# Kernel tuning notes

Hardware: AMD Instinct MI355X
Metric: run time of the kernel (lower is better)

## Reference

```python
import jax, jax.numpy as jnp
import numpy as np

BATCH = 16384
XD = 64      # x_dim
AD = 16      # a_dim
NC = 8       # number of constraints
PEN = 10.0   # relax_penalty
DELTA = 1.0  # class-K coefficient
ITERS = 250  # FISTA iterations for the dual QP (converges to OSQP solution)


def _cbf_forward(a_des, x, A, B, Qc, cc, dc):
    """Batched CBF-QP safety filter.

    Constraints: g_i(x) = 0.5 x^T Qc_i x + cc_i^T x - dc_i  (g_i <= 0 is safe)
    Barrier:     h_i(x) = -g_i(x),  grad_h = -(Qc_i x + cc_i)
    QP:  min ||a - a_des||^2 + PEN * ||s||^2
         s.t. Lg_h a >= -Lf_h - DELTA*h - s,  s >= 0
    Solved exactly (to FISTA tolerance) via the dual:
         min_{lam>=0} 0.5 lam^T M lam - lam^T q,
    with z = [a; s], H = diag(2*1_AD, 2*PEN*1_NC), z = z0 + H^{-1} G^T lam.
    """
    bsz = a_des.shape[0]
    # constraint values and gradients (the 'autograd jacobian' in the original)
    g_x = 0.5 * jnp.einsum('bi,mij,bj->bm', x, Qc, x) + x @ cc.T - dc[None, :]
    h_x = -g_x                                              # [B, NC]
    grad_h = -(jnp.einsum('mij,bj->bmi', Qc, x) + cc[None])  # [B, NC, XD]
    # Lie derivatives
    Lf_h = jnp.einsum('bmi,bij,bj->bm', grad_h, A, x)        # [B, NC]
    Lg_h = jnp.einsum('bmi,bia->bma', grad_h, B)             # [B, NC, AD]
    bvec = -Lf_h - DELTA * h_x                               # rhs: Lg_h a + s >= bvec

    # dual QP setup: G z >= c, G = [[Lg_h, I],[0, I]], c = [bvec; 0]
    Im = jnp.broadcast_to(jnp.eye(NC, dtype=a_des.dtype), (bsz, NC, NC))
    Gtop = jnp.concatenate([Lg_h, Im], axis=2)                    # [B, NC, AD+NC]
    Gbot = jnp.concatenate([jnp.zeros((bsz, NC, AD), a_des.dtype), Im], axis=2)
    G = jnp.concatenate([Gtop, Gbot], axis=1)                     # [B, 2NC, AD+NC]
    dinv = jnp.concatenate([0.5 * jnp.ones(AD, a_des.dtype),
                            jnp.ones(NC, a_des.dtype) / (2.0 * PEN)])
    Mmat = jnp.einsum('bkn,n,bln->bkl', G, dinv, G)               # [B, 2NC, 2NC]
    q = jnp.concatenate([bvec - jnp.einsum('bma,ba->bm', Lg_h, a_des),
                         jnp.zeros((bsz, NC), a_des.dtype)], axis=1)

    # step size 1/L, L = max eigenvalue of M (not differentiated)
    L = jax.lax.stop_gradient(jnp.linalg.eigvalsh(Mmat)[..., -1]) + 1e-6
    t = (1.0 / L)[:, None]

    lam0 = jnp.zeros((bsz, 2 * NC), a_des.dtype)

    def step(carry, _):
        lam, y, tk = carry
        grad = jnp.einsum('bkl,bl->bk', Mmat, y) - q
        lam_new = jnp.maximum(y - t * grad, 0.0)
        tk1 = 0.5 * (1.0 + jnp.sqrt(1.0 + 4.0 * tk * tk))
        y_new = lam_new + ((tk - 1.0) / tk1) * (lam_new - lam)
        return (lam_new, y_new, tk1), None

    (lam, _, _), _ = jax.lax.scan(step, (lam0, lam0, jnp.float32(1.0)), None, length=ITERS)

    # primal recovery: a = a_des + 0.5 * Lg_h^T lam_top
    a_safe = a_des + 0.5 * jnp.einsum('bma,bm->ba', Lg_h, lam[:, :NC])
    return a_safe


def setup_inputs() -> dict:
    key = jax.random.key(0)
    ks = jax.random.split(key, 7)
    a_des = jax.random.normal(ks[0], (BATCH, AD), jnp.float32)
    x = jax.random.normal(ks[1], (BATCH, XD), jnp.float32)
    A = jax.random.normal(ks[2], (BATCH, XD, XD), jnp.float32) * 0.05
    B = jax.random.normal(ks[3], (BATCH, XD, AD), jnp.float32) * 0.1
    R = jax.random.normal(ks[4], (NC, XD, XD), jnp.float32) * 0.05
    Qc = R + jnp.swapaxes(R, 1, 2)  # symmetric quadratic constraint Hessians
    cc = jax.random.normal(ks[5], (NC, XD), jnp.float32) * 0.1
    dc = jax.random.uniform(ks[6], (NC,), jnp.float32) + 0.5
    return {"a_des": a_des, "x": x, "A": A, "B": B, "Qc": Qc, "cc": cc, "dc": dc}


def reference(a_des, x, A, B, Qc, cc, dc):
    return _cbf_forward(a_des, x, A, B, Qc, cc, dc)
```

## Files before the change

kernel.cpp:

```cpp
#include <hip/hip_runtime.h>
#include <cstddef>

#define NBATCH 16384

struct Betas {
  float b[250];
  static constexpr double csqrt(double x) {
    double g = x > 1.0 ? x : 1.0;
    for (int i = 0; i < 64; ++i) g = 0.5 * (g + x / g);
    return g;
  }
  constexpr Betas() : b{} {
    double tk = 1.0;
    for (int i = 0; i < 250; ++i) {
      double tk1 = 0.5 * (1.0 + csqrt(1.0 + 4.0 * tk * tk));
      b[i] = (float)((tk - 1.0) / tk1);
      tk = tk1;
    }
  }
};
__device__ constexpr Betas BETAS{};

__global__ __launch_bounds__(256) void cbf_k1_gh(
    const float* __restrict__ Qc, const float* __restrict__ cc,
    const float* __restrict__ X, float* __restrict__ gh) {
  __shared__ float tile[64 * 132];
  const int tid = threadIdx.x;
  const int e   = tid & 63;
  const int rc  = tid >> 6;
  const int b0  = (blockIdx.x & 255) * 64;
  const int r0  = (blockIdx.x >> 8) * 256;

  float4 xr[16];
  const float4* xp = (const float4*)(X + (size_t)(b0 + e) * 64);
#pragma unroll
  for (int c = 0; c < 16; ++c) xr[c] = xp[c];

  const int rcu = __builtin_amdgcn_readfirstlane(rc);

  for (int p = 0; p < 2; ++p) {
    const int rbase = r0 + p * 128 + rcu * 32;
    const float* wbase = Qc + (size_t)rbase * 64;
#pragma unroll 4
    for (int rl = 0; rl < 32; ++rl) {
      const float4* w = (const float4*)(wbase + rl * 64);
      float a0 = 0.f, a1 = 0.f;
#pragma unroll
      for (int c = 0; c < 16; ++c) {
        float4 wv = w[c];
        a0 = fmaf(wv.x, xr[c].x, a0);
        a1 = fmaf(wv.y, xr[c].y, a1);
        a0 = fmaf(wv.z, xr[c].z, a0);
        a1 = fmaf(wv.w, xr[c].w, a1);
      }
      tile[e * 132 + rc * 32 + rl] = a0 + a1 + cc[rbase + rl];
    }
    __syncthreads();
    {
      const int c  = tid & 31;
      const int bq = tid >> 5;
#pragma unroll
      for (int bp = 0; bp < 8; ++bp) {
        const int bb = bp * 8 + bq;
        float4 v = *(const float4*)&tile[bb * 132 + c * 4];
        *(float4*)(gh + (size_t)(b0 + bb) * 512 + (r0 + p * 128) + c * 4) = v;
      }
    }
    __syncthreads();
  }
}

#define ESTR  1800
#define XOFF  0
#define BVOFF 64
#define BOFF  72
#define GHOFF (72 + 1024)
#define LGOFF (1096 + 544)

__global__ __launch_bounds__(256) void cbf_k2_setup(
    const float* __restrict__ X, const float* __restrict__ Abat,
    const float* __restrict__ Bbat, const float* __restrict__ cc,
    const float* __restrict__ dc, const float* __restrict__ a_des,
    const float* __restrict__ gh, float* __restrict__ S_ws,
    float* __restrict__ LgT_ws, float* __restrict__ qu_ws) {
  __shared__ float smem[4 * ESTR];
  const int tid  = threadIdx.x;
  const int sub  = tid >> 6;
  const int lane = tid & 63;
  const int b    = blockIdx.x * 4 + sub;
  float* sm = smem + sub * ESTR;

  const float xi = X[(size_t)b * 64 + lane];
  sm[XOFF + lane] = xi;
  {
    const float4* bp = (const float4*)(Bbat + (size_t)b * 1024);
#pragma unroll
    for (int n = 0; n < 4; ++n) {
      float4 v = bp[n * 64 + lane];
      *(float4*)&sm[BOFF + n * 256 + lane * 4] = v;
    }
  }
  __syncthreads();

  float ax = 0.f;
  {
    const float4* ap = (const float4*)(Abat + (size_t)b * 4096 + (size_t)lane * 64);
#pragma unroll
    for (int c = 0; c < 16; ++c) {
      float4 av = ap[c];
      float4 xv = *(const float4*)&sm[XOFF + 4 * c];
      ax = fmaf(av.x, xv.x, ax);
      ax = fmaf(av.y, xv.y, ax);
      ax = fmaf(av.z, xv.z, ax);
      ax = fmaf(av.w, xv.w, ax);
    }
  }

#pragma unroll
  for (int m = 0; m < 8; ++m) {
    float ghm = gh[(size_t)b * 512 + m * 64 + lane];
    float ccm = cc[m * 64 + lane];
    sm[GHOFF + m * 68 + lane] = ghm;
    float p1 = xi * ghm;
    float p2 = ax * ghm;
    float p3 = ccm * xi;
#pragma unroll
    for (int s = 1; s < 64; s <<= 1) {
      p1 += __shfl_xor(p1, s);
      p2 += __shfl_xor(p2, s);
      p3 += __shfl_xor(p3, s);
    }
    float g  = 0.5f * (p1 + p3) - dc[m];
    float bv = p2 + g;
    if (lane == 0) sm[BVOFF + m] = bv;
  }
  __syncthreads();

  const int mq  = lane >> 3;
  const int ap2 = lane & 7;
  float acc0 = 0.f, acc1 = 0.f;
#pragma unroll
  for (int c = 0; c < 16; ++c) {
    float4 gv = *(const float4*)&sm[GHOFF + mq * 68 + 4 * c];
#pragma unroll
    for (int n = 0; n < 4; ++n) {
      float2 bv2 = *(const float2*)&sm[BOFF + (4 * c + n) * 16 + 2 * ap2];
      float gvn = (n == 0) ? gv.x : ((n == 1) ? gv.y : ((n == 2) ? gv.z : gv.w));
      acc0 = fmaf(gvn, bv2.x, acc0);
      acc1 = fmaf(gvn, bv2.y, acc1);
    }
  }
  const float lg0 = -acc0, lg1 = -acc1;
  LgT_ws[(size_t)b * 128 + (2 * ap2) * 8 + mq]     = lg0;
  LgT_ws[(size_t)b * 128 + (2 * ap2 + 1) * 8 + mq] = lg1;
  sm[LGOFF + mq * 20 + 2 * ap2]     = lg0;
  sm[LGOFF + mq * 20 + 2 * ap2 + 1] = lg1;
  __syncthreads();

  const int kq = lane >> 3;
  const int lq = lane & 7;
  float s = 0.f;
#pragma unroll
  for (int c = 0; c < 4; ++c) {
    float4 ka = *(const float4*)&sm[LGOFF + kq * 20 + 4 * c];
    float4 la = *(const float4*)&sm[LGOFF + lq * 20 + 4 * c];
    s = fmaf(ka.x, la.x, s);
    s = fmaf(ka.y, la.y, s);
    s = fmaf(ka.z, la.z, s);
    s = fmaf(ka.w, la.w, s);
  }
  S_ws[(size_t)b * 64 + kq * 8 + lq] = 0.5f * s;

  float2 ad2 = *(const float2*)(a_des + (size_t)b * 16 + 2 * lq);
  float2 kg  = *(const float2*)&sm[LGOFF + kq * 20 + 2 * lq];
  float p = kg.x * ad2.x + kg.y * ad2.y;
  p += __shfl_xor(p, 1);
  p += __shfl_xor(p, 2);
  p += __shfl_xor(p, 4);
  float quv = sm[BVOFF + kq] - p;
  if (lq == 0) qu_ws[(size_t)b * 8 + kq] = quv;
}

__global__ __launch_bounds__(256) void cbf_k3_fista(
    const float* __restrict__ S_ws, const float* __restrict__ qu_ws,
    const float* __restrict__ LgT_ws, const float* __restrict__ a_des,
    float* __restrict__ out) {
  const int gt = blockIdx.x * 256 + threadIdx.x;
  const int e  = gt >> 3;
  const int k  = gt & 7;

  const float4* Sp = (const float4*)(S_ws + (size_t)e * 64 + k * 8);
  const float4 sA = Sp[0];
  const float4 sB = Sp[1];
  const float qu = qu_ws[(size_t)e * 8 + k];

#define MV(vv, a0, a1)                              \
  a0 = sA.x * __shfl(vv, 0, 8);                     \
  a1 = sA.y * __shfl(vv, 1, 8);                     \
  a0 = fmaf(sA.z, __shfl(vv, 2, 8), a0);            \
  a1 = fmaf(sA.w, __shfl(vv, 3, 8), a1);            \
  a0 = fmaf(sB.x, __shfl(vv, 4, 8), a0);            \
  a1 = fmaf(sB.y, __shfl(vv, 5, 8), a1);            \
  a0 = fmaf(sB.z, __shfl(vv, 6, 8), a0);            \
  a1 = fmaf(sB.w, __shfl(vv, 7, 8), a1);

  float v = 1.f;
  float a0, a1, sv;
#pragma unroll 4
  for (int it = 0; it < 40; ++it) {
    MV(v, a0, a1);
    sv = a0 + a1;
    float am = fabsf(sv);
    am = fmaxf(am, __shfl_xor(am, 1));
    am = fmaxf(am, __shfl_xor(am, 2));
    am = fmaxf(am, __shfl_xor(am, 4));
    v = sv / fmaxf(am, 1e-30f);
  }
  MV(v, a0, a1);
  sv = a0 + a1;
  float num = v * sv, den = v * v;
  num += __shfl_xor(num, 1); den += __shfl_xor(den, 1);
  num += __shfl_xor(num, 2); den += __shfl_xor(den, 2);
  num += __shfl_xor(num, 4); den += __shfl_xor(den, 4);
  float mu = (num / fmaxf(den, 1e-30f)) * 1.001f;
  mu = fmaxf(mu, 0.f);
  const float lmax = 0.5f * ((0.1f + mu) + sqrtf(fmaf(mu, mu, 0.01f)));
  const float t = 1.0f / (lmax + 1e-6f);

  float yu = 0.f, yv = 0.f, lu = 0.f, lv = 0.f;
#pragma unroll 5
  for (int it = 0; it < 250; ++it) {
    const float beta = BETAS.b[it];
    const float w = 0.05f * (yu + yv);
    MV(yu, a0, a1);
    const float gu = (a0 + a1) + (w - qu);
    const float lun = fmaxf(fmaf(-t, gu, yu), 0.f);
    const float lvn = fmaxf(fmaf(-t, w, yv), 0.f);
    yu = fmaf(beta, lun - lu, lun); lu = lun;
    yv = fmaf(beta, lvn - lv, lvn); lv = lvn;
  }

  const float4* Lp = (const float4*)(LgT_ws + (size_t)e * 128 + k * 16);
  const float4 g0 = Lp[0], g1 = Lp[1], g2 = Lp[2], g3 = Lp[3];
  const float r0[8] = {g0.x, g0.y, g0.z, g0.w, g1.x, g1.y, g1.z, g1.w};
  const float r1[8] = {g2.x, g2.y, g2.z, g2.w, g3.x, g3.y, g3.z, g3.w};
  float o0 = 0.f, o1 = 0.f;
#pragma unroll
  for (int l = 0; l < 8; ++l) {
    const float lamv = __shfl(lu, l, 8);
    o0 = fmaf(r0[l], lamv, o0);
    o1 = fmaf(r1[l], lamv, o1);
  }
  float2 ad = *(const float2*)(a_des + (size_t)e * 16 + 2 * k);
  float2 o;
  o.x = ad.x + 0.5f * o0;
  o.y = ad.y + 0.5f * o1;
  *(float2*)(out + (size_t)e * 16 + 2 * k) = o;
#undef MV
}

extern "C" void kernel_launch(void* const* d_in, const int* in_sizes, int n_in,
                              void* d_out, int out_size, void* d_ws, size_t ws_size,
                              hipStream_t stream) {
  (void)in_sizes; (void)n_in; (void)out_size; (void)ws_size;
  const float* a_des = (const float*)d_in[0];
  const float* x     = (const float*)d_in[1];
  const float* A     = (const float*)d_in[2];
  const float* B     = (const float*)d_in[3];
  const float* Qc    = (const float*)d_in[4];
  const float* cc    = (const float*)d_in[5];
  const float* dc    = (const float*)d_in[6];
  float* out = (float*)d_out;

  float* gh  = (float*)d_ws;
  float* S   = gh  + (size_t)NBATCH * 512;
  float* LgT = S   + (size_t)NBATCH * 64;
  float* qu  = LgT + (size_t)NBATCH * 128;

  hipLaunchKernelGGL(cbf_k1_gh, dim3(512), dim3(256), 0, stream, Qc, cc, x, gh);
  hipLaunchKernelGGL(cbf_k2_setup, dim3(4096), dim3(256), 0, stream,
                     x, A, B, cc, dc, a_des, gh, S, LgT, qu);
  hipLaunchKernelGGL(cbf_k3_fista, dim3(512), dim3(256), 0, stream,
                     S, qu, LgT, a_des, out);
}
```

Measured before the change: 561.2 us.

## Use 4 lanes per QP with DPP broadcasts and coalesce A·x loads

The FISTA kernel now assigns each batch element to 4 lanes instead of 8. Each lane holds two dual rows, and the per-iteration matrix-vector products use DPP quad broadcasts instead of general shuffles, halving the grid. The setup kernel reads A with coalesced float4 loads and reduces the partial dot products across lanes through shared memory, replacing per-lane strided row reads. This trades fewer threads and cheaper cross-lane traffic for more registers per thread and twice the serial work per lane.

```diff
diff --git a/kernel.cpp b/kernel.cpp
--- a/kernel.cpp
+++ b/kernel.cpp
@@ -20,6 +20,12 @@
   }
 };
 __device__ constexpr Betas BETAS{};
+
+template <int CTRL>
+__device__ __forceinline__ float fdpp(float v) {
+  return __int_as_float(
+      __builtin_amdgcn_mov_dpp(__float_as_int(v), CTRL, 0xF, 0xF, true));
+}
 
 __global__ __launch_bounds__(256) void cbf_k1_gh(
     const float* __restrict__ Qc, const float* __restrict__ cc,
@@ -70,12 +76,13 @@
   }
 }
 
-#define ESTR  1800
 #define XOFF  0
 #define BVOFF 64
 #define BOFF  72
 #define GHOFF (72 + 1024)
 #define LGOFF (1096 + 544)
+#define AXOFF (1640 + 160)
+#define ESTR  (1800 + 64)
 
 __global__ __launch_bounds__(256) void cbf_k2_setup(
     const float* __restrict__ X, const float* __restrict__ Abat,
@@ -102,19 +109,24 @@
   }
   __syncthreads();
 
-  float ax = 0.f;
   {
-    const float4* ap = (const float4*)(Abat + (size_t)b * 4096 + (size_t)lane * 64);
-#pragma unroll
-    for (int c = 0; c < 16; ++c) {
-      float4 av = ap[c];
-      float4 xv = *(const float4*)&sm[XOFF + 4 * c];
-      ax = fmaf(av.x, xv.x, ax);
-      ax = fmaf(av.y, xv.y, ax);
-      ax = fmaf(av.z, xv.z, ax);
-      ax = fmaf(av.w, xv.w, ax);
-    }
-  }
+    const float4* ap = (const float4*)(Abat + (size_t)b * 4096);
+    const int cg = lane & 15;
+    const int rg = lane >> 4;
+    const float4 xv = *(const float4*)&sm[XOFF + cg * 4];
+#pragma unroll
+    for (int n = 0; n < 16; ++n) {
+      float4 av = ap[n * 64 + lane];
+      float p = av.x * xv.x + av.y * xv.y + av.z * xv.z + av.w * xv.w;
+      p += __shfl_xor(p, 1);
+      p += __shfl_xor(p, 2);
+      p += __shfl_xor(p, 4);
+      p += __shfl_xor(p, 8);
+      if (cg == 0) sm[AXOFF + n * 4 + rg] = p;
+    }
+  }
+  __syncthreads();
+  const float ax = sm[AXOFF + lane];
 
 #pragma unroll
   for (int m = 0; m < 8; ++m) {
@@ -186,77 +198,91 @@
     const float* __restrict__ LgT_ws, const float* __restrict__ a_des,
     float* __restrict__ out) {
   const int gt = blockIdx.x * 256 + threadIdx.x;
-  const int e  = gt >> 3;
-  const int k  = gt & 7;
-
-  const float4* Sp = (const float4*)(S_ws + (size_t)e * 64 + k * 8);
-  const float4 sA = Sp[0];
-  const float4 sB = Sp[1];
-  const float qu = qu_ws[(size_t)e * 8 + k];
-
-#define MV(vv, a0, a1)                              \
-  a0 = sA.x * __shfl(vv, 0, 8);                     \
-  a1 = sA.y * __shfl(vv, 1, 8);                     \
-  a0 = fmaf(sA.z, __shfl(vv, 2, 8), a0);            \
-  a1 = fmaf(sA.w, __shfl(vv, 3, 8), a1);            \
-  a0 = fmaf(sB.x, __shfl(vv, 4, 8), a0);            \
-  a1 = fmaf(sB.y, __shfl(vv, 5, 8), a1);            \
-  a0 = fmaf(sB.z, __shfl(vv, 6, 8), a0);            \
-  a1 = fmaf(sB.w, __shfl(vv, 7, 8), a1);
-
-  float v = 1.f;
-  float a0, a1, sv;
+  const int e  = gt >> 2;
+  const int q  = gt & 3;
+
+  const float4* Sp = (const float4*)(S_ws + (size_t)e * 64);
+  const float4 sl0 = Sp[q * 2],       sl1 = Sp[q * 2 + 1];
+  const float4 sh0 = Sp[(q + 4) * 2], sh1 = Sp[(q + 4) * 2 + 1];
+  const float qu_lo = qu_ws[(size_t)e * 8 + q];
+  const float qu_hi = qu_ws[(size_t)e * 8 + q + 4];
+
+#define MV(ylo, yhi, alo, ahi) do {                                          \
+    float b0 = fdpp<0x00>(ylo), b1 = fdpp<0x55>(ylo);                        \
+    float b2 = fdpp<0xAA>(ylo), b3 = fdpp<0xFF>(ylo);                        \
+    float b4 = fdpp<0x00>(yhi), b5 = fdpp<0x55>(yhi);                        \
+    float b6 = fdpp<0xAA>(yhi), b7 = fdpp<0xFF>(yhi);                        \
+    float t0 = sl0.x * b0, t1 = sl0.y * b1;                                  \
+    t0 = fmaf(sl0.z, b2, t0); t1 = fmaf(sl0.w, b3, t1);                      \
+    t0 = fmaf(sl1.x, b4, t0); t1 = fmaf(sl1.y, b5, t1);                      \
+    t0 = fmaf(sl1.z, b6, t0); t1 = fmaf(sl1.w, b7, t1);                      \
+    alo = t0 + t1;                                                           \
+    float u0 = sh0.x * b0, u1 = sh0.y * b1;                                  \
+    u0 = fmaf(sh0.z, b2, u0); u1 = fmaf(sh0.w, b3, u1);                      \
+    u0 = fmaf(sh1.x, b4, u0); u1 = fmaf(sh1.y, b5, u1);                      \
+    u0 = fmaf(sh1.z, b6, u0); u1 = fmaf(sh1.w, b7, u1);                      \
+    ahi = u0 + u1;                                                           \
+  } while (0)
+
+  float vl = 1.f, vh = 1.f, svl, svh;
 #pragma unroll 4
   for (int it = 0; it < 40; ++it) {
-    MV(v, a0, a1);
-    sv = a0 + a1;
-    float am = fabsf(sv);
-    am = fmaxf(am, __shfl_xor(am, 1));
-    am = fmaxf(am, __shfl_xor(am, 2));
-    am = fmaxf(am, __shfl_xor(am, 4));
-    v = sv / fmaxf(am, 1e-30f);
-  }
-  MV(v, a0, a1);
-  sv = a0 + a1;
-  float num = v * sv, den = v * v;
-  num += __shfl_xor(num, 1); den += __shfl_xor(den, 1);
-  num += __shfl_xor(num, 2); den += __shfl_xor(den, 2);
-  num += __shfl_xor(num, 4); den += __shfl_xor(den, 4);
-  float mu = (num / fmaxf(den, 1e-30f)) * 1.001f;
-  mu = fmaxf(mu, 0.f);
+    MV(vl, vh, svl, svh);
+    float am = fmaxf(fabsf(svl), fabsf(svh));
+    am = fmaxf(am, fdpp<0xB1>(am));
+    am = fmaxf(am, fdpp<0x4E>(am));
+    float r = 1.f / fmaxf(am, 1e-30f);
+    vl = svl * r; vh = svh * r;
+  }
+  MV(vl, vh, svl, svh);
+  float num = vl * svl + vh * svh;
+  float den = vl * vl + vh * vh;
+  num += fdpp<0xB1>(num); den += fdpp<0xB1>(den);
+  num += fdpp<0x4E>(num); den += fdpp<0x4E>(den);
+  float mu = fmaxf((num / fmaxf(den, 1e-30f)) * 1.001f, 0.f);
   const float lmax = 0.5f * ((0.1f + mu) + sqrtf(fmaf(mu, mu, 0.01f)));
   const float t = 1.0f / (lmax + 1e-6f);
 
-  float yu = 0.f, yv = 0.f, lu = 0.f, lv = 0.f;
+  float yul = 0.f, yuh = 0.f, yvl = 0.f, yvh = 0.f;
+  float lul = 0.f, luh = 0.f, lvl_ = 0.f, lvh = 0.f;
 #pragma unroll 5
   for (int it = 0; it < 250; ++it) {
     const float beta = BETAS.b[it];
-    const float w = 0.05f * (yu + yv);
-    MV(yu, a0, a1);
-    const float gu = (a0 + a1) + (w - qu);
-    const float lun = fmaxf(fmaf(-t, gu, yu), 0.f);
-    const float lvn = fmaxf(fmaf(-t, w, yv), 0.f);
-    yu = fmaf(beta, lun - lu, lun); lu = lun;
-    yv = fmaf(beta, lvn - lv, lvn); lv = lvn;
-  }
-
-  const float4* Lp = (const float4*)(LgT_ws + (size_t)e * 128 + k * 16);
-  const float4 g0 = Lp[0], g1 = Lp[1], g2 = Lp[2], g3 = Lp[3];
-  const float r0[8] = {g0.x, g0.y, g0.z, g0.w, g1.x, g1.y, g1.z, g1.w};
-  const float r1[8] = {g2.x, g2.y, g2.z, g2.w, g3.x, g3.y, g3.z, g3.w};
-  float o0 = 0.f, o1 = 0.f;
-#pragma unroll
-  for (int l = 0; l < 8; ++l) {
-    const float lamv = __shfl(lu, l, 8);
-    o0 = fmaf(r0[l], lamv, o0);
-    o1 = fmaf(r1[l], lamv, o1);
-  }
-  float2 ad = *(const float2*)(a_des + (size_t)e * 16 + 2 * k);
-  float2 o;
-  o.x = ad.x + 0.5f * o0;
-  o.y = ad.y + 0.5f * o1;
-  *(float2*)(out + (size_t)e * 16 + 2 * k) = o;
+    const float wl = 0.05f * (yul + yvl);
+    const float wh = 0.05f * (yuh + yvh);
+    float al, ah;
+    MV(yul, yuh, al, ah);
+    const float gul = al + wl - qu_lo;
+    const float guh = ah + wh - qu_hi;
+    const float lunl = fmaxf(fmaf(-t, gul, yul), 0.f);
+    const float lunh = fmaxf(fmaf(-t, guh, yuh), 0.f);
+    const float lvnl = fmaxf(fmaf(-t, wl, yvl), 0.f);
+    const float lvnh = fmaxf(fmaf(-t, wh, yvh), 0.f);
+    yul = fmaf(beta, lunl - lul, lunl); lul = lunl;
+    yuh = fmaf(beta, lunh - luh, lunh); luh = lunh;
+    yvl = fmaf(beta, lvnl - lvl_, lvnl); lvl_ = lvnl;
+    yvh = fmaf(beta, lvnh - lvh, lvnh); lvh = lvnh;
+  }
 #undef MV
+
+  const float l0 = fdpp<0x00>(lul), l1 = fdpp<0x55>(lul);
+  const float l2 = fdpp<0xAA>(lul), l3 = fdpp<0xFF>(lul);
+  const float l4 = fdpp<0x00>(luh), l5 = fdpp<0x55>(luh);
+  const float l6 = fdpp<0xAA>(luh), l7 = fdpp<0xFF>(luh);
+  const float4* Lp = (const float4*)(LgT_ws + (size_t)e * 128 + q * 32);
+  const float4 ad  = *(const float4*)(a_des + (size_t)e * 16 + q * 4);
+  float o[4];
+#pragma unroll
+  for (int j = 0; j < 4; ++j) {
+    float4 ga = Lp[j * 2], gb = Lp[j * 2 + 1];
+    float s = ga.x * l0 + ga.y * l1 + ga.z * l2 + ga.w * l3
+            + gb.x * l4 + gb.y * l5 + gb.z * l6 + gb.w * l7;
+    o[j] = 0.5f * s;
+  }
+  float4 ov;
+  ov.x = ad.x + o[0]; ov.y = ad.y + o[1];
+  ov.z = ad.z + o[2]; ov.w = ad.w + o[3];
+  *(float4*)(out + (size_t)e * 16 + q * 4) = ov;
 }
 
 extern "C" void kernel_launch(void* const* d_in, const int* in_sizes, int n_in,
@@ -280,6 +306,6 @@
   hipLaunchKernelGGL(cbf_k1_gh, dim3(512), dim3(256), 0, stream, Qc, cc, x, gh);
   hipLaunchKernelGGL(cbf_k2_setup, dim3(4096), dim3(256), 0, stream,
                      x, A, B, cc, dc, a_des, gh, S, LgT, qu);
-  hipLaunchKernelGGL(cbf_k3_fista, dim3(512), dim3(256), 0, stream,
+  hipLaunchKernelGGL(cbf_k3_fista, dim3(256), dim3(256), 0, stream,
                      S, qu, LgT, a_des, out);
 }
```

New measurement: 540.4 us. -3.7%, faster.
